# Kernel tuning notes

Measured on AMD Instinct MI355X. Metric: run time of the kernel, lower is better.

The kernel has to match this reference:

```python
import jax, jax.numpy as jnp
import numpy as np

N, E, IN, H = 20000, 50000, 32, 64


def _lin_init(k, fan_in, shape):
    b = 1.0 / np.sqrt(fan_in)
    return jax.random.uniform(k, shape, jnp.float32, -b, b)


def setup_inputs() -> dict:
    key = jax.random.key(0)
    ks = jax.random.split(key, 16)
    inp = {
        "x": jax.random.normal(ks[0], (N, IN), jnp.float32),
        "edge_index": jax.random.randint(ks[1], (2, E), 0, N, dtype=jnp.int32),
        "edge_attr": jax.random.normal(ks[2], (E, 1, 2), jnp.float32),
        # layer 0: edge MLP 2->H->IN*H, root [IN,H], bias [H]
        "w1_0": _lin_init(ks[3], 2, (2, H)),
        "b1_0": _lin_init(ks[4], 2, (H,)),
        "w2_0": _lin_init(ks[5], H, (H, IN * H)),
        "b2_0": _lin_init(ks[6], H, (IN * H,)),
        "root_0": _lin_init(ks[7], IN, (IN, H)),
        "bias_0": _lin_init(ks[8], IN, (H,)),
        # layer 1: edge MLP 2->H->H*H, root [H,H], bias [H]
        "w1_1": _lin_init(ks[9], 2, (2, H)),
        "b1_1": _lin_init(ks[10], 2, (H,)),
        "w2_1": _lin_init(ks[11], H, (H, H * H)),
        "b2_1": _lin_init(ks[12], H, (H * H,)),
        "root_1": _lin_init(ks[13], H, (H, H)),
        "bias_1": _lin_init(ks[14], H, (H,)),
    }
    return inp


def _nnconv(x, src, dst, ea, w1, b1, w2, b2, root, bias, in_c, out_c):
    # per-edge weight matrices from edge-attr MLP: [E, in_c*out_c]
    h = jax.nn.relu(ea @ w1 + b1) @ w2 + b2
    W = h.reshape(-1, in_c, out_c)                     # [E, in, out]
    msg = jnp.einsum('ei,eio->eo', x[src], W)          # gather + per-edge matmul
    agg = jax.ops.segment_sum(msg, dst, num_segments=x.shape[0])  # scatter-add
    return agg + x @ root + bias                       # add aggr (PyG NNConv, aggr='add')


def reference(x, edge_index, edge_attr,
              w1_0, b1_0, w2_0, b2_0, root_0, bias_0,
              w1_1, b1_1, w2_1, b2_1, root_1, bias_1):
    src, dst = edge_index[0], edge_index[1]
    ea = edge_attr.reshape(edge_attr.shape[0], 2)      # [E, 2]
    x = jax.nn.relu(_nnconv(x, src, dst, ea, w1_0, b1_0, w2_0, b2_0, root_0, bias_0, IN, H))
    x = jax.nn.relu(_nnconv(x, src, dst, ea, w1_1, b1_1, w2_1, b2_1, root_1, bias_1, H, H))
    return x
```

## Files before the change

kernel.cpp:

```cpp
#include <hip/hip_runtime.h>

typedef _Float16 v8h __attribute__((ext_vector_type(8)));
typedef float v16f __attribute__((ext_vector_type(16)));

__global__ void prep_bf_both(const float* __restrict__ w2_0, const float* __restrict__ b2_0,
                             _Float16* __restrict__ BF0,
                             const float* __restrict__ w2_1, const float* __restrict__ b2_1,
                             _Float16* __restrict__ BF1) {
    int idx = blockIdx.x * 256 + threadIdx.x;
    const int n0 = 264 * 512;
    const int n1 = 528 * 512;
    const float* w2; const float* b2; _Float16* BF; int IN, rel;
    if (idx < n0)           { w2 = w2_0; b2 = b2_0; BF = BF0; IN = 32; rel = idx; }
    else if (idx < n0 + n1) { w2 = w2_1; b2 = b2_1; BF = BF1; IN = 64; rel = idx - n0; }
    else return;
    int j = rel & 7, lane = (rel >> 3) & 63, f = rel >> 9;
    int nf = f & 1, kk16 = f >> 1;
    int ln = lane & 31, g2 = lane >> 5;
    int k = kk16 * 16 + g2 * 8 + j;
    int ko = k / IN, i = k - ko * IN;
    int o = nf * 32 + ln;
    float v = (ko < 64) ? w2[ko * (IN * 64) + i * 64 + o]
            : (ko == 64 ? b2[i * 64 + o] : 0.f);
    BF[rel] = (_Float16)v;
}

__global__ void node_root_cvt(const float* __restrict__ x, const float* __restrict__ root,
                              const float* __restrict__ bias, float* __restrict__ agg,
                              _Float16* __restrict__ xb, int N) {
    int idx = blockIdx.x * 256 + threadIdx.x;
    if (idx >= N * 64) return;
    int n = idx >> 6, o = idx & 63;
    float s = bias[o];
    const float* xr = x + (size_t)n * 32;
    #pragma unroll 8
    for (int i = 0; i < 32; ++i) s += xr[i] * root[i * 64 + o];
    agg[idx] = s;
    if (o < 32) xb[n * 32 + o] = (_Float16)xr[o];
}

__global__ void mid_kernel(const float* __restrict__ agg0, const float* __restrict__ root1,
                           const float* __restrict__ bias1, _Float16* __restrict__ x1b,
                           float* __restrict__ agg1, int N) {
    int idx = blockIdx.x * 256 + threadIdx.x;
    if (idx >= N * 64) return;
    int n = idx >> 6, o = idx & 63;
    const float* ar = agg0 + (size_t)n * 64;
    float s = bias1[o];
    #pragma unroll 8
    for (int i = 0; i < 64; ++i) s += fmaxf(ar[i], 0.f) * root1[i * 64 + o];
    agg1[idx] = s;
    x1b[idx] = (_Float16)fmaxf(agg0[idx], 0.f);
}

__global__ void final_relu(const float* __restrict__ agg1, float* __restrict__ out, int n) {
    int idx = blockIdx.x * 256 + threadIdx.x;
    if (idx < n) out[idx] = fmaxf(agg1[idx], 0.f);
}

template<int IN_C>
__global__ __launch_bounds__(256, 3)
void edge_gemm(const float* __restrict__ ea,
               const float* __restrict__ w1, const float* __restrict__ b1,
               const _Float16* __restrict__ xb, const _Float16* __restrict__ BF,
               const int* __restrict__ srcI, const int* __restrict__ dstI,
               float* __restrict__ agg, int E) {
    constexpr int PH  = IN_C / 16;
    constexpr int CPR = IN_C / 8;

    __shared__ __align__(16) _Float16 sh_x[64][IN_C];
    __shared__ _Float16 sh_r1[64][66];
    __shared__ float buf[64][65];
    __shared__ int sh_dst[64];

    int tid = threadIdx.x;
    int ebase = blockIdx.x * 64;
    int valid = E - ebase; if (valid > 64) valid = 64;

    if (tid < 64) {
        sh_dst[tid] = (tid < valid) ? dstI[ebase + tid] : 0;
        sh_r1[tid][64] = (_Float16)1.f;
        sh_r1[tid][65] = (_Float16)0.f;
    }
    for (int i = tid; i < 64 * 64; i += 256) {
        int e = i >> 6, j = i & 63;
        int ge = (e < valid) ? (ebase + e) : ebase;
        float a0 = ea[ge * 2], a1 = ea[ge * 2 + 1];
        sh_r1[e][j] = (_Float16)fmaxf(a0 * w1[j] + a1 * w1[64 + j] + b1[j], 0.f);
    }
    for (int i = tid; i < 64 * CPR; i += 256) {
        int r = i / CPR, c = i - r * CPR;
        int sidx = (r < valid) ? srcI[ebase + r] : 0;
        *(uint4*)&sh_x[r][c * 8] = *(const uint4*)(xb + (size_t)sidx * IN_C + (size_t)c * 8);
    }
    __syncthreads();

    int wv = tid >> 6, lane = tid & 63, ln = lane & 31, g2 = lane >> 5;
    int nf = wv & 1, kh = wv >> 1;

    v8h xs0[PH], xs1[PH];
    #pragma unroll
    for (int p = 0; p < PH; ++p) {
        xs0[p] = *(const v8h*)&sh_x[ln][p * 16 + g2 * 8];
        xs1[p] = *(const v8h*)&sh_x[ln + 32][p * 16 + g2 * 8];
    }

    v16f acc0 = {0,0,0,0,0,0,0,0,0,0,0,0,0,0,0,0};
    v16f acc1 = acc0;

    const uint4* bp = (const uint4*)BF + (size_t)nf * 64 + lane;
    int kb = kh * 33;

    uint4 b[PH], bn[PH];
    auto LD = [&](uint4 (&d)[PH], int ko) {
        #pragma unroll
        for (int p = 0; p < PH; ++p) d[p] = bp[(size_t)(ko * PH + p) * 128];
    };
    auto FM = [&](uint4 (&d)[PH], int ko) {
        _Float16 sv0 = sh_r1[ln][ko];
        _Float16 sv1 = sh_r1[ln + 32][ko];
        #pragma unroll
        for (int p = 0; p < PH; ++p) {
            v8h bb; __builtin_memcpy(&bb, &d[p], 16);
            v8h a0 = xs0[p] * sv0;
            v8h a1 = xs1[p] * sv1;
            acc0 = __builtin_amdgcn_mfma_f32_32x32x16_f16(a0, bb, acc0, 0, 0, 0);
            acc1 = __builtin_amdgcn_mfma_f32_32x32x16_f16(a1, bb, acc1, 0, 0, 0);
        }
    };

    LD(b, kb);
    #pragma unroll 1
    for (int t = 0; t < 16; ++t) {
        LD(bn, kb + 2 * t + 1);
        FM(b,  kb + 2 * t);
        LD(b,  kb + 2 * t + 2);
        FM(bn, kb + 2 * t + 1);
    }
    FM(b, kb + 32);

    int colb = nf * 32 + ln;
    if (kh == 1) {
        #pragma unroll
        for (int r = 0; r < 16; ++r) {
            int row = 4 * g2 + (r & 3) + 8 * (r >> 2);
            buf[row][colb]      = acc0[r];
            buf[row + 32][colb] = acc1[r];
        }
    }
    __syncthreads();
    if (kh == 0) {
        #pragma unroll
        for (int r = 0; r < 16; ++r) {
            int row = 4 * g2 + (r & 3) + 8 * (r >> 2);
            if (row < valid)
                atomicAdd(&agg[(size_t)sh_dst[row] * 64 + colb], acc0[r] + buf[row][colb]);
            int row1 = row + 32;
            if (row1 < valid)
                atomicAdd(&agg[(size_t)sh_dst[row1] * 64 + colb], acc1[r] + buf[row1][colb]);
        }
    }
}

extern "C" void kernel_launch(void* const* d_in, const int* in_sizes, int n_in,
                              void* d_out, int out_size, void* d_ws, size_t ws_size,
                              hipStream_t stream) {
    const float* x      = (const float*)d_in[0];
    const int*   ei     = (const int*)d_in[1];
    const float* ea     = (const float*)d_in[2];
    const float* w1_0   = (const float*)d_in[3];
    const float* b1_0   = (const float*)d_in[4];
    const float* w2_0   = (const float*)d_in[5];
    const float* b2_0   = (const float*)d_in[6];
    const float* root_0 = (const float*)d_in[7];
    const float* bias_0 = (const float*)d_in[8];
    const float* w1_1   = (const float*)d_in[9];
    const float* b1_1   = (const float*)d_in[10];
    const float* w2_1   = (const float*)d_in[11];
    const float* b2_1   = (const float*)d_in[12];
    const float* root_1 = (const float*)d_in[13];
    const float* bias_1 = (const float*)d_in[14];
    float* out = (float*)d_out;

    int N = in_sizes[0] / 32;
    int E = in_sizes[1] / 2;
    const int* srcI = ei;
    const int* dstI = ei + E;

    char* ws = (char*)d_ws;
    size_t off = 0;
    auto carve = [&](size_t bytes) {
        void* p = ws + off;
        off += (bytes + 255) & ~(size_t)255;
        return p;
    };
    _Float16* BF0  = (_Float16*)carve((size_t)264 * 512 * 2);
    _Float16* BF1  = (_Float16*)carve((size_t)528 * 512 * 2);
    _Float16* XB0  = (_Float16*)carve((size_t)N * 32 * 2);
    _Float16* X1B  = (_Float16*)carve((size_t)N * 64 * 2);
    float*    AGG0 = (float*)carve((size_t)N * 64 * 4);
    float*    AGG1 = (float*)carve((size_t)N * 64 * 4);

    int tbf = (264 + 528) * 512;
    prep_bf_both<<<(tbf + 255) / 256, 256, 0, stream>>>(w2_0, b2_0, BF0, w2_1, b2_1, BF1);
    node_root_cvt<<<(N * 64 + 255) / 256, 256, 0, stream>>>(x, root_0, bias_0, AGG0, XB0, N);

    int gblocks = (E + 63) / 64;
    edge_gemm<32><<<gblocks, 256, 0, stream>>>(ea, w1_0, b1_0, XB0, BF0, srcI, dstI, AGG0, E);

    mid_kernel<<<(N * 64 + 255) / 256, 256, 0, stream>>>(AGG0, root_1, bias_1, X1B, AGG1, N);

    edge_gemm<64><<<gblocks, 256, 0, stream>>>(ea, w1_1, b1_1, X1B, BF1, srcI, dstI, AGG1, E);

    final_relu<<<(N * 64 + 255) / 256, 256, 0, stream>>>(AGG1, out, N * 64);
}
```

Baseline: 188.4 us.

## Process 128 edges per block in edge GEMM and fuse prep kernels

Each edge_gemm block now handles 128 edges instead of 64, so every B-fragment load from the shared per-layer weight table feeds four MFMA accumulators instead of two. This halves global reads of the weight table per edge and halves the block count. It costs more registers and shared memory, so the occupancy hint drops from 3 to 2 blocks. The weight-prep kernel and the node root/convert kernel are also merged into one launch to save a kernel launch.

```diff
diff --git a/kernel.cpp b/kernel.cpp
--- a/kernel.cpp
+++ b/kernel.cpp
@@ -3,32 +3,32 @@
 typedef _Float16 v8h __attribute__((ext_vector_type(8)));
 typedef float v16f __attribute__((ext_vector_type(16)));
 
-__global__ void prep_bf_both(const float* __restrict__ w2_0, const float* __restrict__ b2_0,
-                             _Float16* __restrict__ BF0,
-                             const float* __restrict__ w2_1, const float* __restrict__ b2_1,
-                             _Float16* __restrict__ BF1) {
+__global__ void prep_fused(const float* __restrict__ w2_0, const float* __restrict__ b2_0,
+                           _Float16* __restrict__ BF0,
+                           const float* __restrict__ w2_1, const float* __restrict__ b2_1,
+                           _Float16* __restrict__ BF1,
+                           const float* __restrict__ x, const float* __restrict__ root,
+                           const float* __restrict__ bias, float* __restrict__ agg,
+                           _Float16* __restrict__ xb, int N) {
     int idx = blockIdx.x * 256 + threadIdx.x;
     const int n0 = 264 * 512;
     const int n1 = 528 * 512;
-    const float* w2; const float* b2; _Float16* BF; int IN, rel;
-    if (idx < n0)           { w2 = w2_0; b2 = b2_0; BF = BF0; IN = 32; rel = idx; }
-    else if (idx < n0 + n1) { w2 = w2_1; b2 = b2_1; BF = BF1; IN = 64; rel = idx - n0; }
-    else return;
-    int j = rel & 7, lane = (rel >> 3) & 63, f = rel >> 9;
-    int nf = f & 1, kk16 = f >> 1;
-    int ln = lane & 31, g2 = lane >> 5;
-    int k = kk16 * 16 + g2 * 8 + j;
-    int ko = k / IN, i = k - ko * IN;
-    int o = nf * 32 + ln;
-    float v = (ko < 64) ? w2[ko * (IN * 64) + i * 64 + o]
-            : (ko == 64 ? b2[i * 64 + o] : 0.f);
-    BF[rel] = (_Float16)v;
-}
-
-__global__ void node_root_cvt(const float* __restrict__ x, const float* __restrict__ root,
-                              const float* __restrict__ bias, float* __restrict__ agg,
-                              _Float16* __restrict__ xb, int N) {
-    int idx = blockIdx.x * 256 + threadIdx.x;
+    if (idx < n0 + n1) {
+        const float* w2; const float* b2; _Float16* BF; int IN, rel;
+        if (idx < n0) { w2 = w2_0; b2 = b2_0; BF = BF0; IN = 32; rel = idx; }
+        else          { w2 = w2_1; b2 = b2_1; BF = BF1; IN = 64; rel = idx - n0; }
+        int j = rel & 7, lane = (rel >> 3) & 63, f = rel >> 9;
+        int nf = f & 1, kk16 = f >> 1;
+        int ln = lane & 31, g2 = lane >> 5;
+        int k = kk16 * 16 + g2 * 8 + j;
+        int ko = k / IN, i = k - ko * IN;
+        int o = nf * 32 + ln;
+        float v = (ko < 64) ? w2[ko * (IN * 64) + i * 64 + o]
+                : (ko == 64 ? b2[i * 64 + o] : 0.f);
+        BF[rel] = (_Float16)v;
+        return;
+    }
+    idx -= (n0 + n1);
     if (idx >= N * 64) return;
     int n = idx >> 6, o = idx & 63;
     float s = bias[o];
@@ -59,7 +59,7 @@
 }
 
 template<int IN_C>
-__global__ __launch_bounds__(256, 3)
+__global__ __launch_bounds__(256, 2)
 void edge_gemm(const float* __restrict__ ea,
                const float* __restrict__ w1, const float* __restrict__ b1,
                const _Float16* __restrict__ xb, const _Float16* __restrict__ BF,
@@ -68,27 +68,27 @@
     constexpr int PH  = IN_C / 16;
     constexpr int CPR = IN_C / 8;
 
-    __shared__ __align__(16) _Float16 sh_x[64][IN_C];
-    __shared__ _Float16 sh_r1[64][66];
-    __shared__ float buf[64][65];
-    __shared__ int sh_dst[64];
+    __shared__ __align__(16) _Float16 sh_x[128][IN_C];
+    __shared__ _Float16 sh_r1[128][66];
+    __shared__ float buf[128][65];
+    __shared__ int sh_dst[128];
 
     int tid = threadIdx.x;
-    int ebase = blockIdx.x * 64;
-    int valid = E - ebase; if (valid > 64) valid = 64;
-
-    if (tid < 64) {
+    int ebase = blockIdx.x * 128;
+    int valid = E - ebase; if (valid > 128) valid = 128;
+
+    if (tid < 128) {
         sh_dst[tid] = (tid < valid) ? dstI[ebase + tid] : 0;
         sh_r1[tid][64] = (_Float16)1.f;
         sh_r1[tid][65] = (_Float16)0.f;
     }
-    for (int i = tid; i < 64 * 64; i += 256) {
+    for (int i = tid; i < 128 * 64; i += 256) {
         int e = i >> 6, j = i & 63;
         int ge = (e < valid) ? (ebase + e) : ebase;
         float a0 = ea[ge * 2], a1 = ea[ge * 2 + 1];
         sh_r1[e][j] = (_Float16)fmaxf(a0 * w1[j] + a1 * w1[64 + j] + b1[j], 0.f);
     }
-    for (int i = tid; i < 64 * CPR; i += 256) {
+    for (int i = tid; i < 128 * CPR; i += 256) {
         int r = i / CPR, c = i - r * CPR;
         int sidx = (r < valid) ? srcI[ebase + r] : 0;
         *(uint4*)&sh_x[r][c * 8] = *(const uint4*)(xb + (size_t)sidx * IN_C + (size_t)c * 8);
@@ -98,15 +98,17 @@
     int wv = tid >> 6, lane = tid & 63, ln = lane & 31, g2 = lane >> 5;
     int nf = wv & 1, kh = wv >> 1;
 
-    v8h xs0[PH], xs1[PH];
+    v8h xs0[PH], xs1[PH], xs2[PH], xs3[PH];
     #pragma unroll
     for (int p = 0; p < PH; ++p) {
-        xs0[p] = *(const v8h*)&sh_x[ln][p * 16 + g2 * 8];
+        xs0[p] = *(const v8h*)&sh_x[ln     ][p * 16 + g2 * 8];
         xs1[p] = *(const v8h*)&sh_x[ln + 32][p * 16 + g2 * 8];
+        xs2[p] = *(const v8h*)&sh_x[ln + 64][p * 16 + g2 * 8];
+        xs3[p] = *(const v8h*)&sh_x[ln + 96][p * 16 + g2 * 8];
     }
 
     v16f acc0 = {0,0,0,0,0,0,0,0,0,0,0,0,0,0,0,0};
-    v16f acc1 = acc0;
+    v16f acc1 = acc0, acc2 = acc0, acc3 = acc0;
 
     const uint4* bp = (const uint4*)BF + (size_t)nf * 64 + lane;
     int kb = kh * 33;
@@ -117,15 +119,17 @@
         for (int p = 0; p < PH; ++p) d[p] = bp[(size_t)(ko * PH + p) * 128];
     };
     auto FM = [&](uint4 (&d)[PH], int ko) {
-        _Float16 sv0 = sh_r1[ln][ko];
+        _Float16 sv0 = sh_r1[ln     ][ko];
         _Float16 sv1 = sh_r1[ln + 32][ko];
+        _Float16 sv2 = sh_r1[ln + 64][ko];
+        _Float16 sv3 = sh_r1[ln + 96][ko];
         #pragma unroll
         for (int p = 0; p < PH; ++p) {
             v8h bb; __builtin_memcpy(&bb, &d[p], 16);
-            v8h a0 = xs0[p] * sv0;
-            v8h a1 = xs1[p] * sv1;
-            acc0 = __builtin_amdgcn_mfma_f32_32x32x16_f16(a0, bb, acc0, 0, 0, 0);
-            acc1 = __builtin_amdgcn_mfma_f32_32x32x16_f16(a1, bb, acc1, 0, 0, 0);
+            acc0 = __builtin_amdgcn_mfma_f32_32x32x16_f16(xs0[p] * sv0, bb, acc0, 0, 0, 0);
+            acc1 = __builtin_amdgcn_mfma_f32_32x32x16_f16(xs1[p] * sv1, bb, acc1, 0, 0, 0);
+            acc2 = __builtin_amdgcn_mfma_f32_32x32x16_f16(xs2[p] * sv2, bb, acc2, 0, 0, 0);
+            acc3 = __builtin_amdgcn_mfma_f32_32x32x16_f16(xs3[p] * sv3, bb, acc3, 0, 0, 0);
         }
     };
 
@@ -144,8 +148,10 @@
         #pragma unroll
         for (int r = 0; r < 16; ++r) {
             int row = 4 * g2 + (r & 3) + 8 * (r >> 2);
-            buf[row][colb]      = acc0[r];
+            buf[row     ][colb] = acc0[r];
             buf[row + 32][colb] = acc1[r];
+            buf[row + 64][colb] = acc2[r];
+            buf[row + 96][colb] = acc3[r];
         }
     }
     __syncthreads();
@@ -158,6 +164,12 @@
             int row1 = row + 32;
             if (row1 < valid)
                 atomicAdd(&agg[(size_t)sh_dst[row1] * 64 + colb], acc1[r] + buf[row1][colb]);
+            int row2 = row + 64;
+            if (row2 < valid)
+                atomicAdd(&agg[(size_t)sh_dst[row2] * 64 + colb], acc2[r] + buf[row2][colb]);
+            int row3 = row + 96;
+            if (row3 < valid)
+                atomicAdd(&agg[(size_t)sh_dst[row3] * 64 + colb], acc3[r] + buf[row3][colb]);
         }
     }
 }
@@ -201,11 +213,11 @@
     float*    AGG0 = (float*)carve((size_t)N * 64 * 4);
     float*    AGG1 = (float*)carve((size_t)N * 64 * 4);
 
-    int tbf = (264 + 528) * 512;
-    prep_bf_both<<<(tbf + 255) / 256, 256, 0, stream>>>(w2_0, b2_0, BF0, w2_1, b2_1, BF1);
-    node_root_cvt<<<(N * 64 + 255) / 256, 256, 0, stream>>>(x, root_0, bias_0, AGG0, XB0, N);
-
-    int gblocks = (E + 63) / 64;
+    int tprep = (264 + 528) * 512 + N * 64;
+    prep_fused<<<(tprep + 255) / 256, 256, 0, stream>>>(w2_0, b2_0, BF0, w2_1, b2_1, BF1,
+                                                        x, root_0, bias_0, AGG0, XB0, N);
+
+    int gblocks = (E + 127) / 128;
     edge_gemm<32><<<gblocks, 256, 0, stream>>>(ea, w1_0, b1_0, XB0, BF0, srcI, dstI, AGG0, E);
 
     mid_kernel<<<(N * 64 + 255) / 256, 256, 0, stream>>>(AGG0, root_1, bias_1, X1B, AGG1, N);
```

Result: faster. 183.7 us (-2.5%).
